# Kernel optimization log

Measured on AMD Instinct MI355X. Metric: run time of the kernel, lower is better.

## Reference

```python
import jax, jax.numpy as jnp
import numpy as np

DIM = 256
HEADS = 8
DIM_HEAD = 64
INNER = HEADS * DIM_HEAD  # 512
B, H, W = 4, 128, 128


def setup_inputs() -> dict:
    key = jax.random.key(0)
    ks = jax.random.split(key, 7)
    x = jax.random.normal(ks[0], (B, DIM, H, W), dtype=jnp.float32)
    context = jax.random.normal(ks[1], (B, DIM, H, W), dtype=jnp.float32)
    # weights stored as (in, out) so projection is x @ W
    s_in = 1.0 / np.sqrt(DIM)
    s_inner = 1.0 / np.sqrt(INNER)
    Wq = jax.random.uniform(ks[2], (DIM, INNER), jnp.float32, -s_in, s_in)
    Wk = jax.random.uniform(ks[3], (DIM, INNER), jnp.float32, -s_in, s_in)
    Wv = jax.random.uniform(ks[4], (DIM, INNER), jnp.float32, -s_in, s_in)
    Wo = jax.random.uniform(ks[5], (INNER, DIM), jnp.float32, -s_inner, s_inner)
    bo = jax.random.uniform(ks[6], (DIM,), jnp.float32, -s_inner, s_inner)
    return {"x": x, "context": context, "Wq": Wq, "Wk": Wk, "Wv": Wv, "Wo": Wo, "bo": bo}


def reference(x, context, Wq, Wk, Wv, Wo, bo):
    b, c, h, w = x.shape
    n = h * w
    x_flat = x.reshape(b, c, n).transpose(0, 2, 1)          # b n c
    ctx_flat = context.reshape(b, c, n).transpose(0, 2, 1)  # b n c
    # projections; split heads: b n (h d) -> b h n d
    def heads(t):
        return t.reshape(b, n, HEADS, DIM_HEAD).transpose(0, 2, 1, 3)
    q = heads(x_flat @ Wq)
    k = heads(ctx_flat @ Wk)
    v = heads(ctx_flat @ Wv)
    # column-wise softmax over token dim n (axis=-2). NOTE: original module
    # defines scale but never applies it, so we faithfully omit it.
    k = jax.nn.softmax(k, axis=-2)
    cm = jnp.einsum('bhnd,bhne->bhde', k, v)   # small d x e context matrix
    out = jnp.einsum('bhnd,bhde->bhne', q, cm)  # b h n e
    out = out.transpose(0, 2, 1, 3).reshape(b, n, INNER)
    out = out @ Wo + bo
    out = out.transpose(0, 2, 1).reshape(b, c, h, w)
    return x + out
```

## Files before the change

kernel.cpp:

```cpp
#include <hip/hip_runtime.h>

typedef unsigned short u16;
typedef u16   u16x4  __attribute__((ext_vector_type(4)));
typedef u16   u16x8  __attribute__((ext_vector_type(8)));
typedef __bf16 bf16x8 __attribute__((ext_vector_type(8)));
typedef float f32x4  __attribute__((ext_vector_type(4)));

constexpr int BATCH  = 4;
constexpr int CDIM   = 256;
constexpr int NTOK   = 16384;
constexpr int INNERD = 512;

__device__ __forceinline__ u16 f2b(float f) {
  return __builtin_bit_cast(u16, (__bf16)f);
}
__device__ __forceinline__ float b2f(u16 b) {
  return (float)__builtin_bit_cast(__bf16, b);
}

__device__ __forceinline__ void async_ld16(const u16* g, u16* l) {
  __builtin_amdgcn_global_load_lds(
      (const __attribute__((address_space(1))) void*)g,
      (__attribute__((address_space(3))) void*)l, 16, 0, 0);
}

__global__ __launch_bounds__(256) void transpose_cvt(
    const float* __restrict__ x, const float* __restrict__ ctx,
    u16* __restrict__ xt, u16* __restrict__ ct) {
  __shared__ float tile[64][33];
  int zb = blockIdx.z;
  int b = zb >> 1;
  const float* src = (zb & 1) ? ctx : x;
  u16* dst = (zb & 1) ? ct : xt;
  src += (size_t)b * CDIM * NTOK;
  dst += (size_t)b * NTOK * CDIM;
  int n0 = blockIdx.x * 32, c0 = blockIdx.y * 64;
  int tx = threadIdx.x & 31, ty = threadIdx.x >> 5;
#pragma unroll
  for (int i = 0; i < 64; i += 8)
    tile[ty + i][tx] = src[(size_t)(c0 + ty + i) * NTOK + n0 + tx];
  __syncthreads();
  int nl = threadIdx.x >> 3;
  int cl = (threadIdx.x & 7) * 8;
  u16x8 o;
#pragma unroll
  for (int j = 0; j < 8; j++) o[j] = f2b(tile[cl + j][nl]);
  *(u16x8*)&dst[(size_t)(n0 + nl) * CDIM + c0 + cl] = o;
}

__global__ __launch_bounds__(256) void wtrans(
    const float* __restrict__ Wq, const float* __restrict__ Wk, const float* __restrict__ Wv,
    u16* __restrict__ qt, u16* __restrict__ kt, u16* __restrict__ vt) {
  __shared__ float tile[32][33];
  const float* src = blockIdx.z == 0 ? Wq : (blockIdx.z == 1 ? Wk : Wv);
  u16* dst = blockIdx.z == 0 ? qt : (blockIdx.z == 1 ? kt : vt);
  int i0 = blockIdx.x * 32, c0 = blockIdx.y * 32;
  int tx = threadIdx.x & 31, ty = threadIdx.x >> 5;
#pragma unroll
  for (int r = 0; r < 32; r += 8)
    tile[ty + r][tx] = src[(size_t)(c0 + ty + r) * INNERD + i0 + tx];
  __syncthreads();
#pragma unroll
  for (int r = 0; r < 32; r += 8)
    dst[(size_t)(i0 + ty + r) * CDIM + c0 + tx] = f2b(tile[tx][ty + r]);
}

__global__ void zero_f32(float* p, int nelem) {
  int i = blockIdx.x * blockDim.x + threadIdx.x;
  if (i < nelem) p[i] = 0.0f;
}

__global__ __launch_bounds__(256, 2) void proj_ctx(
    const u16* __restrict__ Wkt, const u16* __restrict__ Wvt,
    const u16* __restrict__ ctx_bt, float* __restrict__ cm, float* __restrict__ ksum) {
  int id = blockIdx.x;
  int swz = (id & 7) * 64 + (id >> 3);
  int ig = swz & 3, nc = (swz >> 2) & 31, b = swz >> 7;
  int i0 = ig * 128;
  const u16* Bt = ctx_bt + (size_t)b * NTOK * CDIM;

  __shared__ __align__(16) u16 smem[32768];
  u16* As = smem;
  u16* Bs = smem + 8192;
  u16* Vt = smem;
  u16* Ek = smem + 16384;

  int tid = threadIdx.x, wave = tid >> 6, lane = tid & 63;
  int wm = (wave >> 1) * 64, wn = (wave & 1) * 64;
  int quad = lane >> 4, l16 = lane & 15;
  int srow = lane >> 3, scol = (lane & 7) * 8;

  int hl = wave >> 1, dblk = (wave & 1) * 32;

  u16x8 ov;
#pragma unroll
  for (int t = 0; t < 8; t++) ov[t] = 0x3f80;
  const bf16x8 ones = __builtin_bit_cast(bf16x8, ov);

  f32x4 acc_cm[2][4];
  f32x4 accS[2];
#pragma unroll
  for (int i = 0; i < 2; i++) {
    accS[i] = (f32x4)(0.0f);
#pragma unroll
    for (int j = 0; j < 4; j++) acc_cm[i][j] = (f32x4)(0.0f);
  }

  for (int nt = 0; nt < 4; nt++) {
    int n0 = nc * 512 + nt * 128;
#pragma unroll 1
    for (int kv = 0; kv < 2; kv++) {
      const u16* A = kv ? Wvt : Wkt;
      f32x4 acc[4][4];
#pragma unroll
      for (int i = 0; i < 4; i++)
#pragma unroll
        for (int j = 0; j < 4; j++) acc[i][j] = (f32x4)(0.0f);

      for (int k0 = 0; k0 < CDIM; k0 += 64) {
        __syncthreads();
#pragma unroll
        for (int j = 0; j < 4; j++) {
          int t = wave * 4 + j;
          int row = t * 8 + srow;
          async_ld16(&A [(size_t)(i0 + row) * CDIM + k0 + scol], &As[t * 512]);
          async_ld16(&Bt[(size_t)(n0 + row) * CDIM + k0 + scol], &Bs[t * 512]);
        }
        __syncthreads();
#pragma unroll
        for (int kk = 0; kk < 64; kk += 32) {
          int ko = kk + quad * 8;
          bf16x8 af[4], bfr[4];
#pragma unroll
          for (int m = 0; m < 4; m++)
            af[m] = __builtin_bit_cast(bf16x8, *(const u16x8*)&As[(wm + m * 16 + l16) * 64 + ko]);
#pragma unroll
          for (int e = 0; e < 4; e++)
            bfr[e] = __builtin_bit_cast(bf16x8, *(const u16x8*)&Bs[(wn + e * 16 + l16) * 64 + ko]);
#pragma unroll
          for (int e = 0; e < 4; e++)
#pragma unroll
            for (int m = 0; m < 4; m++)
              acc[e][m] = __builtin_amdgcn_mfma_f32_16x16x32_bf16(bfr[e], af[m], acc[e][m], 0, 0, 0);
        }
      }
      __syncthreads();
      u16* T = kv ? Vt : Ek;
#pragma unroll
      for (int e = 0; e < 4; e++) {
        int nl0 = wn + e * 16 + quad * 4;
#pragma unroll
        for (int m = 0; m < 4; m++) {
          int row = wm + m * 16 + l16;
          u16x4 o;
#pragma unroll
          for (int r = 0; r < 4; r++) {
            float v = acc[e][m][r];
            if (!kv) v = __expf(v);
            o[r] = f2b(v);
          }
          unsigned byt = (unsigned)(row * 256 + nl0 * 2) ^ ((unsigned)(row & 7) << 4);
          *(u16x4*)((char*)T + byt) = o;
        }
      }
    }
    __syncthreads();
#pragma unroll
    for (int kk = 0; kk < 128; kk += 32) {
      int ko = kk + quad * 8;
      bf16x8 ea[2], vb[4];
#pragma unroll
      for (int m2 = 0; m2 < 2; m2++) {
        int row = hl * 64 + dblk + m2 * 16 + l16;
        unsigned byt = (unsigned)(row * 256 + ko * 2) ^ ((unsigned)(row & 7) << 4);
        ea[m2] = __builtin_bit_cast(bf16x8, *(const u16x8*)((char*)Ek + byt));
      }
#pragma unroll
      for (int e2 = 0; e2 < 4; e2++) {
        int row = hl * 64 + e2 * 16 + l16;
        unsigned byt = (unsigned)(row * 256 + ko * 2) ^ ((unsigned)(row & 7) << 4);
        vb[e2] = __builtin_bit_cast(bf16x8, *(const u16x8*)((char*)Vt + byt));
      }
#pragma unroll
      for (int m2 = 0; m2 < 2; m2++) {
        accS[m2] = __builtin_amdgcn_mfma_f32_16x16x32_bf16(ea[m2], ones, accS[m2], 0, 0, 0);
#pragma unroll
        for (int e2 = 0; e2 < 4; e2++)
          acc_cm[m2][e2] = __builtin_amdgcn_mfma_f32_16x16x32_bf16(ea[m2], vb[e2], acc_cm[m2][e2], 0, 0, 0);
      }
    }
  }
  int h = ig * 2 + hl;
  float* cmp = cm + (size_t)(b * 8 + h) * 64 * 64;
#pragma unroll
  for (int m2 = 0; m2 < 2; m2++)
#pragma unroll
    for (int e2 = 0; e2 < 4; e2++)
#pragma unroll
      for (int r = 0; r < 4; r++) {
        int d = dblk + m2 * 16 + quad * 4 + r;
        int e = e2 * 16 + l16;
        atomicAdd(&cmp[d * 64 + e], acc_cm[m2][e2][r]);
      }
  if (l16 == 0) {
#pragma unroll
    for (int m2 = 0; m2 < 2; m2++)
#pragma unroll
      for (int r = 0; r < 4; r++) {
        int d = dblk + m2 * 16 + quad * 4 + r;
        atomicAdd(&ksum[(size_t)b * INNERD + h * 64 + d], accS[m2][r]);
      }
  }
}

__global__ __launch_bounds__(256) void weff_k(
    const float* __restrict__ cm, const float* __restrict__ Wo,
    const float* __restrict__ ksum, float* __restrict__ weff) {
  int bi = blockIdx.x;
  int b = bi >> 9, i = bi & 511, h = i >> 6, d = i & 63;
  const float* cmr = cm + ((size_t)(b * 8 + h) * 64 + d) * 64;
  __shared__ float cs[64];
  if (threadIdx.x < 64) cs[threadIdx.x] = cmr[threadIdx.x];
  __syncthreads();
  float inv = 1.0f / ksum[(size_t)b * INNERD + i];
  int c = threadIdx.x;
  float s = 0.0f;
#pragma unroll 8
  for (int e = 0; e < 64; e++) s += cs[e] * Wo[(size_t)(h * 64 + e) * CDIM + c];
  weff[(size_t)bi * CDIM + c] = s * inv;
}

__global__ __launch_bounds__(256) void gt_k(
    const float* __restrict__ weff, const u16* __restrict__ Wq_t, u16* __restrict__ Gt) {
  int bc = blockIdx.x;
  int b = bc >> 8, c = bc & 255;
  __shared__ float ws[512];
  for (int j = threadIdx.x; j < 512; j += 256)
    ws[j] = weff[((size_t)b * 512 + j) * CDIM + c];
  __syncthreads();
  int cp = threadIdx.x;
  float s = 0.0f;
#pragma unroll 8
  for (int i = 0; i < 512; i++) s += ws[i] * b2f(Wq_t[(size_t)i * CDIM + cp]);
  Gt[(size_t)bc * CDIM + cp] = f2b(s);
}

__global__ __launch_bounds__(256) void final_gemm(
    const u16* __restrict__ Gt, const u16* __restrict__ x_bt,
    const float* __restrict__ x, const float* __restrict__ bo,
    float* __restrict__ out) {
  int id = blockIdx.x;
  int swz = (id & 7) * 128 + (id >> 3);
  int bx = swz & 1, by = (swz >> 1) & 127, b = swz >> 8;
  const u16* A  = Gt + (size_t)b * CDIM * CDIM;
  const u16* Bt = x_bt + (size_t)b * NTOK * CDIM;
  const float* xb = x + (size_t)b * CDIM * NTOK;
  float* ob = out + (size_t)b * CDIM * NTOK;
  int i0 = bx * 128;
  int n0 = by * 128;

  __shared__ __align__(16) u16 As[128 * 64];
  __shared__ __align__(16) u16 Bs[128 * 64];

  int tid = threadIdx.x;
  int wave = tid >> 6, lane = tid & 63;
  int wm = (wave >> 1) * 64, wn = (wave & 1) * 64;
  int quad = lane >> 4, l16 = lane & 15;
  int srow = lane >> 3, scol = (lane & 7) * 8;

  f32x4 acc[4][4];
#pragma unroll
  for (int i = 0; i < 4; i++)
#pragma unroll
    for (int j = 0; j < 4; j++) acc[i][j] = (f32x4)(0.0f);

  for (int k0 = 0; k0 < CDIM; k0 += 64) {
    __syncthreads();
#pragma unroll
    for (int j = 0; j < 4; j++) {
      int t = wave * 4 + j;
      int row = t * 8 + srow;
      async_ld16(&A [(size_t)(i0 + row) * CDIM + k0 + scol], &As[t * 512]);
      async_ld16(&Bt[(size_t)(n0 + row) * CDIM + k0 + scol], &Bs[t * 512]);
    }
    __syncthreads();
#pragma unroll
    for (int kk = 0; kk < 64; kk += 32) {
      int ko = kk + quad * 8;
      bf16x8 af[4], bfr[4];
#pragma unroll
      for (int m = 0; m < 4; m++)
        af[m] = __builtin_bit_cast(bf16x8, *(const u16x8*)&As[(wm + m * 16 + l16) * 64 + ko]);
#pragma unroll
      for (int e = 0; e < 4; e++)
        bfr[e] = __builtin_bit_cast(bf16x8, *(const u16x8*)&Bs[(wn + e * 16 + l16) * 64 + ko]);
#pragma unroll
      for (int e = 0; e < 4; e++)
#pragma unroll
        for (int m = 0; m < 4; m++)
          acc[e][m] = __builtin_amdgcn_mfma_f32_16x16x32_bf16(bfr[e], af[m], acc[e][m], 0, 0, 0);
    }
  }
#pragma unroll
  for (int e = 0; e < 4; e++) {
    int nb = n0 + wn + e * 16 + quad * 4;
#pragma unroll
    for (int m = 0; m < 4; m++) {
      int c = i0 + wm + m * 16 + l16;
      f32x4 xv = *(const f32x4*)&xb[(size_t)c * NTOK + nb];
      f32x4 r;
      float bc = bo[c];
#pragma unroll
      for (int t = 0; t < 4; t++) r[t] = acc[e][m][t] + xv[t] + bc;
      *(f32x4*)&ob[(size_t)c * NTOK + nb] = r;
    }
  }
}

extern "C" void kernel_launch(void* const* d_in, const int* in_sizes, int n_in,
                              void* d_out, int out_size, void* d_ws, size_t ws_size,
                              hipStream_t stream) {
  const float* x   = (const float*)d_in[0];
  const float* ctx = (const float*)d_in[1];
  const float* Wq  = (const float*)d_in[2];
  const float* Wk  = (const float*)d_in[3];
  const float* Wv  = (const float*)d_in[4];
  const float* Wo  = (const float*)d_in[5];
  const float* bo  = (const float*)d_in[6];
  float* out = (float*)d_out;

  char* ws = (char*)d_ws;
  u16* ctx_bt = (u16*)ws;  ws += (size_t)BATCH * NTOK * CDIM * 2;
  u16* x_bt   = (u16*)ws;  ws += (size_t)BATCH * NTOK * CDIM * 2;
  u16* Wq_t   = (u16*)ws;  ws += (size_t)INNERD * CDIM * 2;
  u16* Wk_t   = (u16*)ws;  ws += (size_t)INNERD * CDIM * 2;
  u16* Wv_t   = (u16*)ws;  ws += (size_t)INNERD * CDIM * 2;
  float* cm   = (float*)ws; ws += (size_t)BATCH * 8 * 64 * 64 * 4;
  float* ksum = (float*)ws; ws += (size_t)BATCH * INNERD * 4;
  float* weff = (float*)ws; ws += (size_t)BATCH * INNERD * CDIM * 4;
  u16* Gt     = (u16*)ws;  ws += (size_t)BATCH * CDIM * CDIM * 2;

  const int nzero = BATCH * 8 * 64 * 64 + BATCH * INNERD;

  transpose_cvt<<<dim3(NTOK / 32, CDIM / 64, BATCH * 2), 256, 0, stream>>>(x, ctx, x_bt, ctx_bt);
  wtrans<<<dim3(INNERD / 32, CDIM / 32, 3), 256, 0, stream>>>(Wq, Wk, Wv, Wq_t, Wk_t, Wv_t);
  zero_f32<<<(nzero + 255) / 256, 256, 0, stream>>>(cm, nzero);
  proj_ctx<<<dim3(512), 256, 0, stream>>>(Wk_t, Wv_t, ctx_bt, cm, ksum);
  weff_k<<<BATCH * INNERD, 256, 0, stream>>>(cm, Wo, ksum, weff);
  gt_k<<<BATCH * CDIM, 256, 0, stream>>>(weff, Wq_t, Gt);
  final_gemm<<<dim3(1024), 256, 0, stream>>>(Gt, x_bt, x, bo, out);
}
```

Before: 333.3 us.

## Merge prep kernels and double-buffer LDS loads in projection and final GEMMs

Folds the activation transpose, weight transpose and zero-fill into one launch to cut launch overhead. proj_ctx and final_gemm now use a K=32 double-buffered LDS stage, so the next slice's async global-to-LDS loads are issued before the current slice's MFMAs. In proj_ctx the K and V projections become a single 16-step pipeline with the exp/store of K done mid-loop. Each K-step now carries less work per barrier, and the buffer aliasing between Ek/Vt and the staging buffers needs care.

```diff
diff --git a/kernel.cpp b/kernel.cpp
--- a/kernel.cpp
+++ b/kernel.cpp
@@ -24,50 +24,53 @@
       (__attribute__((address_space(3))) void*)l, 16, 0, 0);
 }
 
-__global__ __launch_bounds__(256) void transpose_cvt(
+constexpr int ZERO_N = BATCH * 8 * 64 * 64 + BATCH * INNERD;
+__global__ __launch_bounds__(256) void prep(
     const float* __restrict__ x, const float* __restrict__ ctx,
-    u16* __restrict__ xt, u16* __restrict__ ct) {
+    const float* __restrict__ Wq, const float* __restrict__ Wk, const float* __restrict__ Wv,
+    u16* __restrict__ xt, u16* __restrict__ ct,
+    u16* __restrict__ qt, u16* __restrict__ kt, u16* __restrict__ vt,
+    float* __restrict__ zbuf) {
   __shared__ float tile[64][33];
-  int zb = blockIdx.z;
-  int b = zb >> 1;
-  const float* src = (zb & 1) ? ctx : x;
-  u16* dst = (zb & 1) ? ct : xt;
-  src += (size_t)b * CDIM * NTOK;
-  dst += (size_t)b * NTOK * CDIM;
-  int n0 = blockIdx.x * 32, c0 = blockIdx.y * 64;
-  int tx = threadIdx.x & 31, ty = threadIdx.x >> 5;
-#pragma unroll
-  for (int i = 0; i < 64; i += 8)
-    tile[ty + i][tx] = src[(size_t)(c0 + ty + i) * NTOK + n0 + tx];
-  __syncthreads();
-  int nl = threadIdx.x >> 3;
-  int cl = (threadIdx.x & 7) * 8;
-  u16x8 o;
-#pragma unroll
-  for (int j = 0; j < 8; j++) o[j] = f2b(tile[cl + j][nl]);
-  *(u16x8*)&dst[(size_t)(n0 + nl) * CDIM + c0 + cl] = o;
-}
-
-__global__ __launch_bounds__(256) void wtrans(
-    const float* __restrict__ Wq, const float* __restrict__ Wk, const float* __restrict__ Wv,
-    u16* __restrict__ qt, u16* __restrict__ kt, u16* __restrict__ vt) {
-  __shared__ float tile[32][33];
-  const float* src = blockIdx.z == 0 ? Wq : (blockIdx.z == 1 ? Wk : Wv);
-  u16* dst = blockIdx.z == 0 ? qt : (blockIdx.z == 1 ? kt : vt);
-  int i0 = blockIdx.x * 32, c0 = blockIdx.y * 32;
-  int tx = threadIdx.x & 31, ty = threadIdx.x >> 5;
-#pragma unroll
-  for (int r = 0; r < 32; r += 8)
-    tile[ty + r][tx] = src[(size_t)(c0 + ty + r) * INNERD + i0 + tx];
-  __syncthreads();
-#pragma unroll
-  for (int r = 0; r < 32; r += 8)
-    dst[(size_t)(i0 + ty + r) * CDIM + c0 + tx] = f2b(tile[tx][ty + r]);
-}
-
-__global__ void zero_f32(float* p, int nelem) {
-  int i = blockIdx.x * blockDim.x + threadIdx.x;
-  if (i < nelem) p[i] = 0.0f;
+  int id = blockIdx.x;
+  if (id < 16384) {
+    int bx = id & 511, by = (id >> 9) & 3, zb = id >> 11;
+    int b = zb >> 1;
+    const float* src = (zb & 1) ? ctx : x;
+    u16* dst = (zb & 1) ? ct : xt;
+    src += (size_t)b * CDIM * NTOK;
+    dst += (size_t)b * NTOK * CDIM;
+    int n0 = bx * 32, c0 = by * 64;
+    int tx = threadIdx.x & 31, ty = threadIdx.x >> 5;
+#pragma unroll
+    for (int i = 0; i < 64; i += 8)
+      tile[ty + i][tx] = src[(size_t)(c0 + ty + i) * NTOK + n0 + tx];
+    __syncthreads();
+    int nl = threadIdx.x >> 3;
+    int cl = (threadIdx.x & 7) * 8;
+    u16x8 o;
+#pragma unroll
+    for (int j = 0; j < 8; j++) o[j] = f2b(tile[cl + j][nl]);
+    *(u16x8*)&dst[(size_t)(n0 + nl) * CDIM + c0 + cl] = o;
+  } else if (id < 16768) {
+    int idw = id - 16384;
+    int bx = idw & 15, by = (idw >> 4) & 7, bz = idw >> 7;
+    float (*t2)[33] = (float(*)[33])tile;
+    const float* src = bz == 0 ? Wq : (bz == 1 ? Wk : Wv);
+    u16* dst = bz == 0 ? qt : (bz == 1 ? kt : vt);
+    int i0 = bx * 32, c0 = by * 32;
+    int tx = threadIdx.x & 31, ty = threadIdx.x >> 5;
+#pragma unroll
+    for (int r = 0; r < 32; r += 8)
+      t2[ty + r][tx] = src[(size_t)(c0 + ty + r) * INNERD + i0 + tx];
+    __syncthreads();
+#pragma unroll
+    for (int r = 0; r < 32; r += 8)
+      dst[(size_t)(i0 + ty + r) * CDIM + c0 + tx] = f2b(t2[tx][ty + r]);
+  } else {
+    int i = (id - 16768) * 256 + threadIdx.x;
+    if (i < ZERO_N) zbuf[i] = 0.0f;
+  }
 }
 
 __global__ __launch_bounds__(256, 2) void proj_ctx(
@@ -80,15 +83,13 @@
   const u16* Bt = ctx_bt + (size_t)b * NTOK * CDIM;
 
   __shared__ __align__(16) u16 smem[32768];
-  u16* As = smem;
-  u16* Bs = smem + 8192;
+  u16* Ek = smem + 16384;
   u16* Vt = smem;
-  u16* Ek = smem + 16384;
 
   int tid = threadIdx.x, wave = tid >> 6, lane = tid & 63;
   int wm = (wave >> 1) * 64, wn = (wave & 1) * 64;
   int quad = lane >> 4, l16 = lane & 15;
-  int srow = lane >> 3, scol = (lane & 7) * 8;
+  int sr = lane >> 2, sc = (lane & 3) * 8;
 
   int hl = wave >> 1, dblk = (wave & 1) * 32;
 
@@ -106,62 +107,82 @@
     for (int j = 0; j < 4; j++) acc_cm[i][j] = (f32x4)(0.0f);
   }
 
+  auto stage = [&](int p, int kv, int ks, int n0) {
+    int k0 = ks * 32;
+    const u16* Asrc = kv ? Wvt : Wkt;
+#pragma unroll
+    for (int j = 0; j < 4; j++) {
+      int c = wave * 4 + j;
+      if (c < 8) {
+        int row = c * 16 + sr;
+        async_ld16(&Asrc[(size_t)(i0 + row) * CDIM + k0 + sc], &smem[p * 8192 + c * 512]);
+      } else {
+        int cb = c - 8, row = cb * 16 + sr;
+        async_ld16(&Bt[(size_t)(n0 + row) * CDIM + k0 + sc], &smem[p * 8192 + 4096 + cb * 512]);
+      }
+    }
+  };
+
   for (int nt = 0; nt < 4; nt++) {
     int n0 = nc * 512 + nt * 128;
-#pragma unroll 1
-    for (int kv = 0; kv < 2; kv++) {
-      const u16* A = kv ? Wvt : Wkt;
-      f32x4 acc[4][4];
-#pragma unroll
-      for (int i = 0; i < 4; i++)
-#pragma unroll
-        for (int j = 0; j < 4; j++) acc[i][j] = (f32x4)(0.0f);
-
-      for (int k0 = 0; k0 < CDIM; k0 += 64) {
-        __syncthreads();
-#pragma unroll
-        for (int j = 0; j < 4; j++) {
-          int t = wave * 4 + j;
-          int row = t * 8 + srow;
-          async_ld16(&A [(size_t)(i0 + row) * CDIM + k0 + scol], &As[t * 512]);
-          async_ld16(&Bt[(size_t)(n0 + row) * CDIM + k0 + scol], &Bs[t * 512]);
+    __syncthreads();
+    stage(0, 0, 0, n0);
+    __syncthreads();
+
+    f32x4 acc[4][4];
+#pragma unroll
+    for (int i = 0; i < 4; i++)
+#pragma unroll
+      for (int j = 0; j < 4; j++) acc[i][j] = (f32x4)(0.0f);
+
+#pragma unroll 2
+    for (int s = 0; s < 16; s++) {
+      int p = s & 1;
+      if (s < 15) { int s1 = s + 1; stage(p ^ 1, s1 >> 3, s1 & 7, n0); }
+      const u16* As = &smem[p * 8192];
+      const u16* Bs = &smem[p * 8192 + 4096];
+      bf16x8 af[4], bfr[4];
+#pragma unroll
+      for (int m = 0; m < 4; m++)
+        af[m] = __builtin_bit_cast(bf16x8, *(const u16x8*)&As[(wm + m * 16 + l16) * 32 + quad * 8]);
+#pragma unroll
+      for (int e = 0; e < 4; e++)
+        bfr[e] = __builtin_bit_cast(bf16x8, *(const u16x8*)&Bs[(wn + e * 16 + l16) * 32 + quad * 8]);
+#pragma unroll
+      for (int e = 0; e < 4; e++)
+#pragma unroll
+        for (int m = 0; m < 4; m++)
+          acc[e][m] = __builtin_amdgcn_mfma_f32_16x16x32_bf16(bfr[e], af[m], acc[e][m], 0, 0, 0);
+
+      if (s == 7) {
+#pragma unroll
+        for (int e = 0; e < 4; e++) {
+          int nl0 = wn + e * 16 + quad * 4;
+#pragma unroll
+          for (int m = 0; m < 4; m++) {
+            int row = wm + m * 16 + l16;
+            u16x4 ok;
+#pragma unroll
+            for (int r = 0; r < 4; r++) ok[r] = f2b(__expf(acc[e][m][r]));
+            unsigned byt = (unsigned)(row * 256 + nl0 * 2) ^ ((unsigned)(row & 7) << 4);
+            *(u16x4*)((char*)Ek + byt) = ok;
+            acc[e][m] = (f32x4)(0.0f);
+          }
         }
-        __syncthreads();
-#pragma unroll
-        for (int kk = 0; kk < 64; kk += 32) {
-          int ko = kk + quad * 8;
-          bf16x8 af[4], bfr[4];
-#pragma unroll
-          for (int m = 0; m < 4; m++)
-            af[m] = __builtin_bit_cast(bf16x8, *(const u16x8*)&As[(wm + m * 16 + l16) * 64 + ko]);
-#pragma unroll
-          for (int e = 0; e < 4; e++)
-            bfr[e] = __builtin_bit_cast(bf16x8, *(const u16x8*)&Bs[(wn + e * 16 + l16) * 64 + ko]);
-#pragma unroll
-          for (int e = 0; e < 4; e++)
-#pragma unroll
-            for (int m = 0; m < 4; m++)
-              acc[e][m] = __builtin_amdgcn_mfma_f32_16x16x32_bf16(bfr[e], af[m], acc[e][m], 0, 0, 0);
-        }
       }
       __syncthreads();
-      u16* T = kv ? Vt : Ek;
-#pragma unroll
-      for (int e = 0; e < 4; e++) {
-        int nl0 = wn + e * 16 + quad * 4;
-#pragma unroll
-        for (int m = 0; m < 4; m++) {
-          int row = wm + m * 16 + l16;
-          u16x4 o;
-#pragma unroll
-          for (int r = 0; r < 4; r++) {
-            float v = acc[e][m][r];
-            if (!kv) v = __expf(v);
-            o[r] = f2b(v);
-          }
-          unsigned byt = (unsigned)(row * 256 + nl0 * 2) ^ ((unsigned)(row & 7) << 4);
-          *(u16x4*)((char*)T + byt) = o;
-        }
+    }
+#pragma unroll
+    for (int e = 0; e < 4; e++) {
+      int nl0 = wn + e * 16 + quad * 4;
+#pragma unroll
+      for (int m = 0; m < 4; m++) {
+        int row = wm + m * 16 + l16;
+        u16x4 ovv;
+#pragma unroll
+        for (int r = 0; r < 4; r++) ovv[r] = f2b(acc[e][m][r]);
+        unsigned byt = (unsigned)(row * 256 + nl0 * 2) ^ ((unsigned)(row & 7) << 4);
+        *(u16x4*)((char*)Vt + byt) = ovv;
       }
     }
     __syncthreads();
@@ -259,14 +280,28 @@
   int i0 = bx * 128;
   int n0 = by * 128;
 
-  __shared__ __align__(16) u16 As[128 * 64];
-  __shared__ __align__(16) u16 Bs[128 * 64];
+  __shared__ __align__(16) u16 smem2[16384];
 
   int tid = threadIdx.x;
   int wave = tid >> 6, lane = tid & 63;
   int wm = (wave >> 1) * 64, wn = (wave & 1) * 64;
   int quad = lane >> 4, l16 = lane & 15;
-  int srow = lane >> 3, scol = (lane & 7) * 8;
+  int sr = lane >> 2, sc = (lane & 3) * 8;
+
+  auto stage = [&](int p, int ks) {
+    int k0 = ks * 32;
+#pragma unroll
+    for (int j = 0; j < 4; j++) {
+      int c = wave * 4 + j;
+      if (c < 8) {
+        int row = c * 16 + sr;
+        async_ld16(&A[(size_t)(i0 + row) * CDIM + k0 + sc], &smem2[p * 8192 + c * 512]);
+      } else {
+        int cb = c - 8, row = cb * 16 + sr;
+        async_ld16(&Bt[(size_t)(n0 + row) * CDIM + k0 + sc], &smem2[p * 8192 + 4096 + cb * 512]);
+      }
+    }
+  };
 
   f32x4 acc[4][4];
 #pragma unroll
@@ -274,32 +309,27 @@
 #pragma unroll
     for (int j = 0; j < 4; j++) acc[i][j] = (f32x4)(0.0f);
 
-  for (int k0 = 0; k0 < CDIM; k0 += 64) {
-    __syncthreads();
-#pragma unroll
-    for (int j = 0; j < 4; j++) {
-      int t = wave * 4 + j;
-      int row = t * 8 + srow;
-      async_ld16(&A [(size_t)(i0 + row) * CDIM + k0 + scol], &As[t * 512]);
-      async_ld16(&Bt[(size_t)(n0 + row) * CDIM + k0 + scol], &Bs[t * 512]);
-    }
-    __syncthreads();
-#pragma unroll
-    for (int kk = 0; kk < 64; kk += 32) {
-      int ko = kk + quad * 8;
-      bf16x8 af[4], bfr[4];
+  stage(0, 0);
+  __syncthreads();
+#pragma unroll 2
+  for (int s = 0; s < 8; s++) {
+    int p = s & 1;
+    if (s < 7) stage(p ^ 1, s + 1);
+    const u16* As = &smem2[p * 8192];
+    const u16* Bs = &smem2[p * 8192 + 4096];
+    bf16x8 af[4], bfr[4];
+#pragma unroll
+    for (int m = 0; m < 4; m++)
+      af[m] = __builtin_bit_cast(bf16x8, *(const u16x8*)&As[(wm + m * 16 + l16) * 32 + quad * 8]);
+#pragma unroll
+    for (int e = 0; e < 4; e++)
+      bfr[e] = __builtin_bit_cast(bf16x8, *(const u16x8*)&Bs[(wn + e * 16 + l16) * 32 + quad * 8]);
+#pragma unroll
+    for (int e = 0; e < 4; e++)
 #pragma unroll
       for (int m = 0; m < 4; m++)
-        af[m] = __builtin_bit_cast(bf16x8, *(const u16x8*)&As[(wm + m * 16 + l16) * 64 + ko]);
-#pragma unroll
-      for (int e = 0; e < 4; e++)
-        bfr[e] = __builtin_bit_cast(bf16x8, *(const u16x8*)&Bs[(wn + e * 16 + l16) * 64 + ko]);
-#pragma unroll
-      for (int e = 0; e < 4; e++)
-#pragma unroll
-        for (int m = 0; m < 4; m++)
-          acc[e][m] = __builtin_amdgcn_mfma_f32_16x16x32_bf16(bfr[e], af[m], acc[e][m], 0, 0, 0);
-    }
+        acc[e][m] = __builtin_amdgcn_mfma_f32_16x16x32_bf16(bfr[e], af[m], acc[e][m], 0, 0, 0);
+    if (s < 7) __syncthreads();
   }
 #pragma unroll
   for (int e = 0; e < 4; e++) {
@@ -340,11 +370,8 @@
   float* weff = (float*)ws; ws += (size_t)BATCH * INNERD * CDIM * 4;
   u16* Gt     = (u16*)ws;  ws += (size_t)BATCH * CDIM * CDIM * 2;
 
-  const int nzero = BATCH * 8 * 64 * 64 + BATCH * INNERD;
-
-  transpose_cvt<<<dim3(NTOK / 32, CDIM / 64, BATCH * 2), 256, 0, stream>>>(x, ctx, x_bt, ctx_bt);
-  wtrans<<<dim3(INNERD / 32, CDIM / 32, 3), 256, 0, stream>>>(Wq, Wk, Wv, Wq_t, Wk_t, Wv_t);
-  zero_f32<<<(nzero + 255) / 256, 256, 0, stream>>>(cm, nzero);
+  prep<<<dim3(17288), 256, 0, stream>>>(x, ctx, Wq, Wk, Wv, x_bt, ctx_bt,
+                                        Wq_t, Wk_t, Wv_t, cm );
   proj_ctx<<<dim3(512), 256, 0, stream>>>(Wk_t, Wv_t, ctx_bt, cm, ksum);
   weff_k<<<BATCH * INNERD, 256, 0, stream>>>(cm, Wo, ksum, weff);
   gt_k<<<BATCH * CDIM, 256, 0, stream>>>(weff, Wq_t, Gt);
```

Result: faster. 306.7 us (-8.0%).
